# Kernel optimization log

Measured on AMD Instinct MI355X. Metric: run time of the kernel, lower is better.

## Reference

```python
import jax, jax.numpy as jnp
import numpy as np

B, L, D, A = 64, 512, 512, 8


def setup_inputs() -> dict:
    key = jax.random.key(0)
    ks = jax.random.split(key, 7)
    H = jax.random.normal(ks[0], (B, L, D), dtype=jnp.float32)
    user_embedding = jax.random.normal(ks[1], (B, D), dtype=jnp.float32)
    # xavier_normal-ish scales
    s2d = (2.0 / (2 * D + D)) ** 0.5
    sb = (2.0 / (1 + D)) ** 0.5
    sa = (2.0 / (A + D)) ** 0.5
    asp_vs_d = jax.random.normal(ks[2], (A, D), dtype=jnp.float32) * sa
    W_map = jax.random.normal(ks[3], (A, 2 * D, D), dtype=jnp.float32) * s2d
    b_map = jax.random.normal(ks[4], (A, D), dtype=jnp.float32) * sb
    W_proj = jax.random.normal(ks[5], (A, 2 * D, D), dtype=jnp.float32) * s2d
    b_proj = jax.random.normal(ks[6], (A, D), dtype=jnp.float32) * sb
    return {"H": H, "user_embedding": user_embedding, "asp_vs_d": asp_vs_d,
            "W_map": W_map, "b_map": b_map, "W_proj": W_proj, "b_proj": b_proj}


def reference(H, user_embedding, asp_vs_d, W_map, b_map, W_proj, b_proj):
    b, l, d = H.shape
    a = asp_vs_d.shape[0]
    # User repeated along length, concat on feature dim -> (B, L, 2D)
    User = jnp.broadcast_to(user_embedding[:, None, :], (b, l, d))
    Batch = jnp.concatenate([H, User], axis=2)
    # Batched per-aspect gated linear: (A, B, L, D) == torch.cat(list, dim=0).view(A,B,L,D)
    gate = jax.nn.sigmoid(jnp.einsum('blk,akd->abld', Batch, W_map) + b_map[:, None, None, :])
    proj = jnp.einsum('blk,akd->abld', Batch, W_proj) + b_proj[:, None, None, :]
    map_asp = gate * proj  # (A, B, L, D)
    # NOTE: original does a raw contiguous .reshape(B, L, A, D) (NOT a transpose);
    # replicate faithfully.
    item_asp = map_asp.reshape(b, l, a, d)
    # attention over the length axis
    scores = jnp.sum(item_asp * asp_vs_d, axis=3) + 1e-24  # (B, L, A)
    attn = jax.nn.softmax(scores, axis=1)
    out = jnp.sum(item_asp * attn[..., None], axis=1)  # (B, A, D)
    # dropout is identity in eval mode
    return out
```

## Files before the change

### kernel.cpp

```cpp
#include <hip/hip_runtime.h>
#include <hip/hip_bf16.h>

typedef unsigned short u16;
typedef u16   u16x4 __attribute__((ext_vector_type(4)));
typedef u16   u16x8 __attribute__((ext_vector_type(8)));
typedef short s16x8 __attribute__((ext_vector_type(8)));
typedef float f32x4 __attribute__((ext_vector_type(4)));

#define NB   64
#define NL   512
#define ND   512
#define NA   8
#define K2   1024
#define KH   512
#define MROWS 32768

__device__ __forceinline__ float b2f(u16 u) {
    unsigned int x = ((unsigned int)u) << 16;
    return __uint_as_float(x);
}
__device__ __forceinline__ u16 f2b(float f) {
    unsigned int x = __float_as_uint(f);
    unsigned int r = (x + 0x7fffu + ((x >> 16) & 1u)) >> 16;
    return (u16)r;
}

__device__ __forceinline__ int permc(int k) {
    int ks  = k >> 6;
    int kr  = k & 63;
    int kk  = kr >> 5;
    int k32 = kr & 31;
    int h   = k32 >> 4;
    int rem = k32 & 15;
    int g   = rem >> 2;
    int e0  = rem & 3;
    return ks * 64 + kk * 32 + g * 8 + h * 4 + e0;
}

__device__ __forceinline__ void gload16(const u16* g, u16* l) {
    __builtin_amdgcn_global_load_lds(
        (const __attribute__((address_space(1))) unsigned int*)g,
        (__attribute__((address_space(3))) unsigned int*)l, 16, 0, 0);
}

#define PREP_BB 4096
#define PREP_WT 2048
#define PREP_UM 512

__global__ __launch_bounds__(256) void prep_k(
    const float* __restrict__ H, u16* __restrict__ Bt,
    const float* __restrict__ Wmf, const float* __restrict__ Wpf,
    u16* __restrict__ Wm, u16* __restrict__ Wp,
    const float* __restrict__ U, float* __restrict__ uM, float* __restrict__ uP) {
    __shared__ float shp[5120];
    int bid = blockIdx.x;
    int t = threadIdx.x;

    if (bid < PREP_BB) {
        size_t stride = (size_t)PREP_BB * 256;
        for (size_t idx = (size_t)bid * 256 + t; idx < (size_t)MROWS * 128; idx += stride) {
            int r  = (int)(idx >> 7);
            int c  = ((int)idx & 127) << 2;
            int ks = c >> 6;
            int w64 = c & 63;
            int cq = w64 >> 3;
            int h  = (w64 >> 2) & 1;
            int kbase = ks * 64 + (cq >> 2) * 32 + (cq & 3) * 4 + h * 16;
            f32x4 v = *(const f32x4*)(H + (size_t)r * ND + kbase);
            u16x4 o;
            o[0] = f2b(v[0]); o[1] = f2b(v[1]); o[2] = f2b(v[2]); o[3] = f2b(v[3]);
            *(u16x4*)(Bt + (size_t)r * KH + c) = o;
        }
    } else if (bid < PREP_BB + PREP_WT) {
        int b2 = bid - PREP_BB;
        float (*ld)[65] = (float(*)[65])shp;
        int kt  = b2 & 15;
        int dt  = (b2 >> 4) & 7;
        int a   = (b2 >> 7) & 7;
        int mat = b2 >> 10;
        const float* W = mat ? Wpf : Wmf;
        u16* Wt = mat ? Wp : Wm;
        int k0 = kt * 32, d0 = dt * 64;
        #pragma unroll
        for (int it = 0; it < 8; ++it) {
            int lin = it * 256 + t;
            int i = lin >> 6, j = lin & 63;
            ld[i][j] = W[((size_t)a * K2 + k0 + i) * ND + d0 + j];
        }
        __syncthreads();
        #pragma unroll
        for (int it = 0; it < 8; ++it) {
            int lin = it * 256 + t;
            int dl = lin >> 5, kl = lin & 31;
            int k = k0 + kl;
            Wt[((size_t)a * ND + d0 + dl) * KH + permc(k)] = f2b(ld[kl][dl]);
        }
    } else {
        int b2 = bid - PREP_BB - PREP_WT;
        int a   = b2 & 7;
        int mat = (b2 >> 3) & 1;
        int cg  = (b2 >> 4) & 7;
        int bs  = b2 >> 7;
        const float* W = mat ? Wpf : Wmf;
        float* uX = mat ? uP : uM;
        float* ul = shp;
        float* wl = shp + 1024;
        int c = t & 63, bq = t >> 6;

        float acc[4] = {0.0f, 0.0f, 0.0f, 0.0f};
        for (int kt = 0; kt < 8; ++kt) {
            __syncthreads();
            #pragma unroll
            for (int it = 0; it < 16; ++it) {
                int idx = it * 256 + t;
                wl[idx] = W[((size_t)a * K2 + 512 + kt * 64 + (idx >> 6)) * ND + cg * 64 + (idx & 63)];
            }
            #pragma unroll
            for (int it = 0; it < 4; ++it) {
                int idx = it * 256 + t;
                ul[idx] = U[(size_t)(bs * 16 + (idx >> 6)) * ND + kt * 64 + (idx & 63)];
            }
            __syncthreads();
            #pragma unroll
            for (int k4 = 0; k4 < 16; ++k4) {
                f32x4 uv[4];
                #pragma unroll
                for (int bi = 0; bi < 4; ++bi)
                    uv[bi] = *(const f32x4*)&ul[(bq * 4 + bi) * 64 + k4 * 4];
                #pragma unroll
                for (int e = 0; e < 4; ++e) {
                    float wv = wl[(k4 * 4 + e) * 64 + c];
                    #pragma unroll
                    for (int bi = 0; bi < 4; ++bi)
                        acc[bi] += uv[bi][e] * wv;
                }
            }
        }
        #pragma unroll
        for (int bi = 0; bi < 4; ++bi)
            uX[((size_t)a * NB + bs * 16 + bq * 4 + bi) * ND + cg * 64 + c] = acc[bi];
    }
}

#define BAR()    do { __builtin_amdgcn_sched_barrier(0); \
                      __builtin_amdgcn_s_barrier(); \
                      __builtin_amdgcn_sched_barrier(0); } while (0)
#define WAITV(n) do { asm volatile("s_waitcnt vmcnt(" #n ")" ::: "memory"); \
                      __builtin_amdgcn_sched_barrier(0); } while (0)
#define PRIO1    __builtin_amdgcn_s_setprio(1);
#define PRIO0    __builtin_amdgcn_s_setprio(0);

#define A_OFF  0
#define M_OFF  8192
#define P_OFF  16384
#define TST    136

#define RDA(B_) { _Pragma("unroll") for (int i_ = 0; i_ < 4; ++i_) \
    af[i_] = *(const s16x8*)(pA + (B_) * 4096 + i_ * 512); }
#define RDM(B_) { fm[0] = *(const s16x8*)(pM + (B_) * 4096); \
                  fm[1] = *(const s16x8*)(pM + (B_) * 4096 + 512); }
#define RDP(B_) { fp[0] = *(const s16x8*)(pP + (B_) * 4096); \
                  fp[1] = *(const s16x8*)(pP + (B_) * 4096 + 512); }

#define MMAM { _Pragma("unroll") for (int i_ = 0; i_ < 4; ++i_) \
    _Pragma("unroll") for (int j_ = 0; j_ < 2; ++j_) \
        accM[i_][j_] = __builtin_amdgcn_mfma_f32_16x16x32_bf16( \
            af[i_], fm[j_], accM[i_][j_], 0, 0, 0); }
#define MMAP { _Pragma("unroll") for (int i_ = 0; i_ < 4; ++i_) \
    _Pragma("unroll") for (int j_ = 0; j_ < 2; ++j_) \
        accP[i_][j_] = __builtin_amdgcn_mfma_f32_16x16x32_bf16( \
            af[i_], fp[j_], accP[i_][j_], 0, 0, 0); }

#define STEP(CUR, T) { \
    stA((CUR) ^ 1, (T) + 1); stM((CUR) ^ 1, (T) + 1); stP((CUR) ^ 1, (T) + 1); \
    RDA(CUR) RDM(CUR) \
    PRIO1 MMAM PRIO0 \
    RDP(CUR) \
    PRIO1 MMAP PRIO0 \
    WAITV(0); BAR(); }

__global__ __launch_bounds__(512, 4) void gemm8_k(
    const u16* __restrict__ Bt, const u16* __restrict__ Wm, const u16* __restrict__ Wp,
    const float* __restrict__ bm, const float* __restrict__ bp,
    const float* __restrict__ uM, const float* __restrict__ uP,
    const float* __restrict__ asp,
    u16* __restrict__ item, float* __restrict__ scorep,
    int a0, int log2na, int nwg) {
    __shared__ u16 smem[24576];

    int bid = blockIdx.x;
    int chunk = nwg >> 3;
    int b = (bid & 7) * chunk + (bid >> 3);
    int nt = b & 3;
    int al = (b >> 2) & ((1 << log2na) - 1);
    int mt = b >> (2 + log2na);
    int a  = a0 + al;

    int tid = threadIdx.x;
    int lane = tid & 63;
    int w  = tid >> 6;
    int wr = w >> 2;
    int wc = w & 3;
    int g = lane >> 4, r15 = lane & 15;

    const u16* Abase = Bt + (size_t)(mt * 128) * KH;
    const u16* Mbase = Wm + ((size_t)a * ND + nt * 128) * KH;
    const u16* Pbase = Wp + ((size_t)a * ND + nt * 128) * KH;

    int ps = (g ^ (r15 & 3) ^ ((r15 >> 2) & 3)) << 3;
    const u16* pA = &smem[A_OFF + (wr * 64 + r15) * 32 + ps];
    const u16* pM = &smem[M_OFF + (wc * 32 + r15) * 32 + ps];
    const u16* pP = &smem[P_OFF + (wc * 32 + r15) * 32 + ps];

    int srow = tid >> 2, sq = tid & 3;
    int qsw = (sq ^ (srow & 3) ^ ((srow >> 2) & 3)) << 3;
    auto stA = [&](int buf, int ks) {
        gload16(Abase + (size_t)srow * KH + ks * 32 + qsw,
                &smem[A_OFF + buf * 4096 + srow * 32 + sq * 8]);
    };
    auto stM = [&](int buf, int ks) {
        gload16(Mbase + (size_t)srow * KH + ks * 32 + qsw,
                &smem[M_OFF + buf * 4096 + srow * 32 + sq * 8]);
    };
    auto stP = [&](int buf, int ks) {
        gload16(Pbase + (size_t)srow * KH + ks * 32 + qsw,
                &smem[P_OFF + buf * 4096 + srow * 32 + sq * 8]);
    };

    f32x4 accM[4][2], accP[4][2];
    #pragma unroll
    for (int i = 0; i < 4; ++i)
        #pragma unroll
        for (int j = 0; j < 2; ++j) { accM[i][j] = 0.0f; accP[i][j] = 0.0f; }

    s16x8 af[4], fm[2], fp[2];

    stA(0, 0); stM(0, 0); stP(0, 0);
    WAITV(0); BAR();

    for (int t = 0; t < 14; t += 2) {
        STEP(0, t)
        STEP(1, t + 1)
    }
    STEP(0, 14)

    {
        RDA(1) RDM(1)
        PRIO1 MMAM PRIO0
        RDP(1)
        PRIO1 MMAP PRIO0
    }

    BAR();
    {
        int gc0 = nt * 128 + wc * 32 + r15;
        int gc1 = gc0 + 16;
        int bix = mt >> 2;
        size_t ub = ((size_t)a * NB + bix) * ND;
        float bmv0 = bm[a * ND + gc0] + uM[ub + gc0];
        float bmv1 = bm[a * ND + gc1] + uM[ub + gc1];
        float bpv0 = bp[a * ND + gc0] + uP[ub + gc0];
        float bpv1 = bp[a * ND + gc1] + uP[ub + gc1];
        int col0 = wc * 32 + r15;
        #pragma unroll
        for (int i = 0; i < 4; ++i) {
            int row0 = wr * 64 + i * 16 + g * 4;
            #pragma unroll
            for (int jj = 0; jj < 4; ++jj) {
                float m0 = accM[i][0][jj] + bmv0;
                float p0 = accP[i][0][jj] + bpv0;
                float v0 = p0 * __builtin_amdgcn_rcpf(1.0f + __expf(-m0));
                float m1 = accM[i][1][jj] + bmv1;
                float p1 = accP[i][1][jj] + bpv1;
                float v1 = p1 * __builtin_amdgcn_rcpf(1.0f + __expf(-m1));
                unsigned int pk;
                asm("v_cvt_pk_bf16_f32 %0, %1, %2" : "=v"(pk) : "v"(v0), "v"(v1));
                smem[(row0 + jj) * TST + col0]      = (u16)pk;
                smem[(row0 + jj) * TST + col0 + 16] = (u16)(pk >> 16);
            }
        }
    }
    BAR();
    {
        #pragma unroll
        for (int q = 0; q < 4; ++q) {
            int cid = q * 512 + tid;
            int row_l = cid >> 4;
            int c8 = (cid & 15) << 3;
            u16x8 tv = *(const u16x8*)&smem[row_l * TST + c8];
            int rowg = mt * 128 + row_l;
            int a2 = rowg & 7;
            int colg8 = nt * 128 + c8;
            f32x4 w0 = *(const f32x4*)&asp[a2 * ND + colg8];
            f32x4 w1 = *(const f32x4*)&asp[a2 * ND + colg8 + 4];
            float s = b2f(tv[0]) * w0[0] + b2f(tv[1]) * w0[1]
                    + b2f(tv[2]) * w0[2] + b2f(tv[3]) * w0[3]
                    + b2f(tv[4]) * w1[0] + b2f(tv[5]) * w1[1]
                    + b2f(tv[6]) * w1[2] + b2f(tv[7]) * w1[3];
            *(u16x8*)(item + ((size_t)al * MROWS + rowg) * ND + colg8) = tv;
            s += __shfl_xor(s, 1);
            s += __shfl_xor(s, 2);
            s += __shfl_xor(s, 4);
            s += __shfl_xor(s, 8);
            if ((tid & 15) == 0)
                scorep[((size_t)al * MROWS + rowg) * 4 + nt] = s;
        }
    }
}

__global__ __launch_bounds__(512) void attn_out_k(
    const u16* __restrict__ item, const float* __restrict__ scorep,
    float* __restrict__ out, int b0) {
    __shared__ float attn[512];
    __shared__ float red[512];
    int t = threadIdx.x;
    int ds = blockIdx.x & 7;
    int ap = (blockIdx.x >> 3) & 7;
    int bl = blockIdx.x >> 6;
    int bg = b0 + bl;

    size_t R = (size_t)bl * 4096 + (size_t)t * 8 + ap;
    f32x4 q = *(const f32x4*)(scorep + R * 4);
    float s = (q[0] + q[1]) + (q[2] + q[3]);

    red[t] = s;
    __syncthreads();
    for (int off = 256; off > 0; off >>= 1) {
        if (t < off) red[t] = fmaxf(red[t], red[t + off]);
        __syncthreads();
    }
    float mx = red[0];
    __syncthreads();
    float p = __expf(s - mx);
    red[t] = p;
    __syncthreads();
    for (int off = 256; off > 0; off >>= 1) {
        if (t < off) red[t] += red[t + off];
        __syncthreads();
    }
    float inv = 1.0f / red[0];
    attn[t] = p * inv;
    __syncthreads();

    int lg = t >> 6, c = t & 63;
    const u16* base = item + ((size_t)bl * 4096 + ap) * ND + ds * 64 + c;
    float acc = 0.0f;
    #pragma unroll 4
    for (int l = lg; l < 512; l += 8)
        acc += attn[l] * b2f(base[(size_t)l * 8 * ND]);
    red[t] = acc;
    __syncthreads();
    if (t < 64) {
        float o = 0.0f;
        #pragma unroll
        for (int k = 0; k < 8; ++k) o += red[k * 64 + t];
        out[((size_t)bg * NA + ap) * ND + ds * 64 + t] = o;
    }
}

extern "C" void kernel_launch(void* const* d_in, const int* in_sizes, int n_in,
                              void* d_out, int out_size, void* d_ws, size_t ws_size,
                              hipStream_t stream) {
    const float* H   = (const float*)d_in[0];
    const float* U   = (const float*)d_in[1];
    const float* asp = (const float*)d_in[2];
    const float* Wmf = (const float*)d_in[3];
    const float* bmf = (const float*)d_in[4];
    const float* Wpf = (const float*)d_in[5];
    const float* bpf = (const float*)d_in[6];
    float* out = (float*)d_out;

    char* ws = (char*)d_ws;
    const size_t BT_BYTES = (size_t)MROWS * KH * 2;
    const size_t WT_BYTES = (size_t)NA * ND * KH * 2;
    const size_t U_BYTES  = (size_t)NA * NB * ND * 4;
    u16*   Bt = (u16*)(ws);
    u16*   Wm = (u16*)(ws + BT_BYTES);
    u16*   Wp = (u16*)(ws + BT_BYTES + WT_BYTES);
    float* uM = (float*)(ws + BT_BYTES + 2 * WT_BYTES);
    float* uP = (float*)(ws + BT_BYTES + 2 * WT_BYTES + U_BYTES);
    size_t fixed = BT_BYTES + 2 * WT_BYTES + 2 * U_BYTES;
    const size_t ITEM_PER_ASPECT  = (size_t)MROWS * ND * 2;
    const size_t SCORE_PER_ASPECT = (size_t)MROWS * 4 * 4;
    size_t avail = (ws_size > fixed) ? (ws_size - fixed) : 0;
    int na = (int)(avail / (ITEM_PER_ASPECT + SCORE_PER_ASPECT));
    if (na > NA) na = NA;
    if (na < 1) na = 1;
    int log2na = 0;
    while ((2 << log2na) <= na) ++log2na;
    na = 1 << log2na;
    u16*   item   = (u16*)(ws + fixed);
    float* scorep = (float*)(ws + fixed + (size_t)na * ITEM_PER_ASPECT);

    prep_k<<<PREP_BB + PREP_WT + PREP_UM, 256, 0, stream>>>(
        H, Bt, Wmf, Wpf, Wm, Wp, U, uM, uP);

    for (int a0 = 0; a0 < NA; a0 += na) {
        int n = (na < NA - a0) ? na : (NA - a0);
        gemm8_k<<<n * 1024, 512, 0, stream>>>(Bt, Wm, Wp, bmf, bpf, uM, uP, asp,
                                              item, scorep, a0, log2na, n * 1024);
        attn_out_k<<<n * 512, 512, 0, stream>>>(item, scorep, out, a0 * 8);
    }
}
```

Measured before the change: 422.8 us.

## Double K-step to 64 with single-buffered weight tiles and register prefetch

After: 994.7 us. 135% more time.

```diff
diff --git a/kernel.cpp b/kernel.cpp
--- a/kernel.cpp
+++ b/kernel.cpp
@@ -147,36 +147,43 @@
                       __builtin_amdgcn_sched_barrier(0); } while (0)
 #define WAITV(n) do { asm volatile("s_waitcnt vmcnt(" #n ")" ::: "memory"); \
                       __builtin_amdgcn_sched_barrier(0); } while (0)
+#define LGKM0()  do { asm volatile("s_waitcnt lgkmcnt(0)" ::: "memory"); \
+                      __builtin_amdgcn_sched_barrier(0); } while (0)
 #define PRIO1    __builtin_amdgcn_s_setprio(1);
 #define PRIO0    __builtin_amdgcn_s_setprio(0);
 
 #define A_OFF  0
-#define M_OFF  8192
-#define P_OFF  16384
+#define M_OFF  16384
+#define P_OFF  24576
 #define TST    136
 
-#define RDA(B_) { _Pragma("unroll") for (int i_ = 0; i_ < 4; ++i_) \
-    af[i_] = *(const s16x8*)(pA + (B_) * 4096 + i_ * 512); }
-#define RDM(B_) { fm[0] = *(const s16x8*)(pM + (B_) * 4096); \
-                  fm[1] = *(const s16x8*)(pM + (B_) * 4096 + 512); }
-#define RDP(B_) { fp[0] = *(const s16x8*)(pP + (B_) * 4096); \
-                  fp[1] = *(const s16x8*)(pP + (B_) * 4096 + 512); }
-
-#define MMAM { _Pragma("unroll") for (int i_ = 0; i_ < 4; ++i_) \
+#define RDA(B_) { _Pragma("unroll") for (int i_ = 0; i_ < 4; ++i_) { \
+    af[i_ * 2 + 0] = *(const s16x8*)(pA0 + (B_) * 8192 + i_ * 1024); \
+    af[i_ * 2 + 1] = *(const s16x8*)(pA1 + (B_) * 8192 + i_ * 1024); } }
+#define RDB() { \
+    fm[0] = *(const s16x8*)(pM0); fm[1] = *(const s16x8*)(pM1); \
+    fm[2] = *(const s16x8*)(pM0 + 1024); fm[3] = *(const s16x8*)(pM1 + 1024); \
+    fp[0] = *(const s16x8*)(pP0); fp[1] = *(const s16x8*)(pP1); \
+    fp[2] = *(const s16x8*)(pP0 + 1024); fp[3] = *(const s16x8*)(pP1 + 1024); }
+
+#define MMA_M { _Pragma("unroll") for (int kk_ = 0; kk_ < 2; ++kk_) \
+    _Pragma("unroll") for (int i_ = 0; i_ < 4; ++i_) \
     _Pragma("unroll") for (int j_ = 0; j_ < 2; ++j_) \
         accM[i_][j_] = __builtin_amdgcn_mfma_f32_16x16x32_bf16( \
-            af[i_], fm[j_], accM[i_][j_], 0, 0, 0); }
-#define MMAP { _Pragma("unroll") for (int i_ = 0; i_ < 4; ++i_) \
+            af[i_ * 2 + kk_], fm[j_ * 2 + kk_], accM[i_][j_], 0, 0, 0); }
+#define MMA_P { _Pragma("unroll") for (int kk_ = 0; kk_ < 2; ++kk_) \
+    _Pragma("unroll") for (int i_ = 0; i_ < 4; ++i_) \
     _Pragma("unroll") for (int j_ = 0; j_ < 2; ++j_) \
         accP[i_][j_] = __builtin_amdgcn_mfma_f32_16x16x32_bf16( \
-            af[i_], fp[j_], accP[i_][j_], 0, 0, 0); }
+            af[i_ * 2 + kk_], fp[j_ * 2 + kk_], accP[i_][j_], 0, 0, 0); }
 
 #define STEP(CUR, T) { \
-    stA((CUR) ^ 1, (T) + 1); stM((CUR) ^ 1, (T) + 1); stP((CUR) ^ 1, (T) + 1); \
-    RDA(CUR) RDM(CUR) \
-    PRIO1 MMAM PRIO0 \
-    RDP(CUR) \
-    PRIO1 MMAP PRIO0 \
+    stA((CUR) ^ 1, (T) + 1); \
+    RDA(CUR) RDB() \
+    LGKM0(); BAR(); \
+    stM((T) + 1); stP((T) + 1); \
+    PRIO1 MMA_M PRIO0 \
+    PRIO1 MMA_P PRIO0 \
     WAITV(0); BAR(); }
 
 __global__ __launch_bounds__(512, 4) void gemm8_k(
@@ -186,7 +193,7 @@
     const float* __restrict__ asp,
     u16* __restrict__ item, float* __restrict__ scorep,
     int a0, int log2na, int nwg) {
-    __shared__ u16 smem[24576];
+    __shared__ u16 smem[32768];
 
     int bid = blockIdx.x;
     int chunk = nwg >> 3;
@@ -207,24 +214,40 @@
     const u16* Mbase = Wm + ((size_t)a * ND + nt * 128) * KH;
     const u16* Pbase = Wp + ((size_t)a * ND + nt * 128) * KH;
 
-    int ps = (g ^ (r15 & 3) ^ ((r15 >> 2) & 3)) << 3;
-    const u16* pA = &smem[A_OFF + (wr * 64 + r15) * 32 + ps];
-    const u16* pM = &smem[M_OFF + (wc * 32 + r15) * 32 + ps];
-    const u16* pP = &smem[P_OFF + (wc * 32 + r15) * 32 + ps];
-
-    int srow = tid >> 2, sq = tid & 3;
-    int qsw = (sq ^ (srow & 3) ^ ((srow >> 2) & 3)) << 3;
+    int s0 = g ^ (r15 & 7);
+    int s1 = (4 + g) ^ (r15 & 7);
+    const u16* pA0 = &smem[A_OFF + (wr * 64 + r15) * 64 + s0 * 8];
+    const u16* pA1 = &smem[A_OFF + (wr * 64 + r15) * 64 + s1 * 8];
+    const u16* pM0 = &smem[M_OFF + (wc * 32 + r15) * 64 + s0 * 8];
+    const u16* pM1 = &smem[M_OFF + (wc * 32 + r15) * 64 + s1 * 8];
+    const u16* pP0 = &smem[P_OFF + (wc * 32 + r15) * 64 + s0 * 8];
+    const u16* pP1 = &smem[P_OFF + (wc * 32 + r15) * 64 + s1 * 8];
+
+    int srow = tid >> 3, sq = tid & 7;
+    int qsw = sq ^ (srow & 7);
     auto stA = [&](int buf, int ks) {
-        gload16(Abase + (size_t)srow * KH + ks * 32 + qsw,
-                &smem[A_OFF + buf * 4096 + srow * 32 + sq * 8]);
+        #pragma unroll
+        for (int rnd = 0; rnd < 2; ++rnd) {
+            int row = rnd * 64 + srow;
+            gload16(Abase + (size_t)row * KH + ks * 64 + qsw * 8,
+                    &smem[A_OFF + buf * 8192 + row * 64 + sq * 8]);
+        }
     };
-    auto stM = [&](int buf, int ks) {
-        gload16(Mbase + (size_t)srow * KH + ks * 32 + qsw,
-                &smem[M_OFF + buf * 4096 + srow * 32 + sq * 8]);
+    auto stM = [&](int ks) {
+        #pragma unroll
+        for (int rnd = 0; rnd < 2; ++rnd) {
+            int row = rnd * 64 + srow;
+            gload16(Mbase + (size_t)row * KH + ks * 64 + qsw * 8,
+                    &smem[M_OFF + row * 64 + sq * 8]);
+        }
     };
-    auto stP = [&](int buf, int ks) {
-        gload16(Pbase + (size_t)srow * KH + ks * 32 + qsw,
-                &smem[P_OFF + buf * 4096 + srow * 32 + sq * 8]);
+    auto stP = [&](int ks) {
+        #pragma unroll
+        for (int rnd = 0; rnd < 2; ++rnd) {
+            int row = rnd * 64 + srow;
+            gload16(Pbase + (size_t)row * KH + ks * 64 + qsw * 8,
+                    &smem[P_OFF + row * 64 + sq * 8]);
+        }
     };
 
     f32x4 accM[4][2], accP[4][2];
@@ -233,22 +256,21 @@
         #pragma unroll
         for (int j = 0; j < 2; ++j) { accM[i][j] = 0.0f; accP[i][j] = 0.0f; }
 
-    s16x8 af[4], fm[2], fp[2];
-
-    stA(0, 0); stM(0, 0); stP(0, 0);
+    s16x8 af[8], fm[4], fp[4];
+
+    stA(0, 0); stM(0); stP(0);
     WAITV(0); BAR();
 
-    for (int t = 0; t < 14; t += 2) {
+    for (int t = 0; t < 6; t += 2) {
         STEP(0, t)
         STEP(1, t + 1)
     }
-    STEP(0, 14)
+    STEP(0, 6)
 
     {
-        RDA(1) RDM(1)
-        PRIO1 MMAM PRIO0
-        RDP(1)
-        PRIO1 MMAP PRIO0
+        RDA(1) RDB()
+        PRIO1 MMA_M PRIO0
+        PRIO1 MMA_P PRIO0
     }
 
     BAR();
```
